# Optimization experiments

Hardware: AMD Instinct MI355X
Metric: run time of the kernel (lower is better)

The kernel has to match this reference:

```python
import jax, jax.numpy as jnp
import numpy as np
from jax import lax

C, K, EMB = 10, 32, 32
B, H, W = 32, 128, 128
DIRS = ((-1, 0), (1, 0), (0, -1), (0, 1))  # up, down, left, right


def _shift(x, dh, dw):
    # shift (B,H,W,...) by (dh,dw) with zero fill; x[b,h,w] <- x[b,h+dh,w+dw]
    pad = [(0, 0), (max(dh, 0), max(-dh, 0)), (max(dw, 0), max(-dw, 0))] + [(0, 0)] * (x.ndim - 3)
    xp = jnp.pad(x, pad)
    h0, w0 = max(-dh, 0), max(-dw, 0)
    return lax.dynamic_slice_in_dim(lax.dynamic_slice_in_dim(xp, h0, x.shape[1], 1), w0, x.shape[2], 2)


def conv(x, w, b):
    y = lax.conv_general_dilated(x, w, (1, 1), 'SAME',
                                 dimension_numbers=('NHWC', 'HWIO', 'NHWC'))
    return y + b


def small_cnn(x, w1, b1, w2, b2, w3, b3):
    x = jax.nn.relu(conv(x, w1, b1))
    x = jax.nn.relu(conv(x, w2, b2))
    return conv(x, w3, b3)


def neighbor_affinity(phi, tau=0.5):
    # phi: (B,H,W,D) -> w: (B,H,W,4) Gaussian feature affinity to 4 neighbors
    ones = jnp.ones(phi.shape[:3] + (1,), phi.dtype)
    ws = []
    for dh, dw in DIRS:
        nb = _shift(phi, dh, dw)
        valid = _shift(ones, dh, dw)[..., 0]
        d2 = jnp.sum((phi - nb) ** 2, axis=-1)
        ws.append(jnp.exp(-d2 / tau) * valid)
    return jnp.stack(ws, axis=-1)


def init_seeds_soft(Bv, Hv, Wv, Kv, dtype=jnp.float32):
    # K seeds on a gh x gw grid; soft assignment by squared distance
    gh = 4
    gw = Kv // gh
    sh = (jnp.arange(gh, dtype=dtype) + 0.5) * (Hv / gh)
    sw = (jnp.arange(gw, dtype=dtype) + 0.5) * (Wv / gw)
    seed_h = jnp.repeat(sh, gw)  # (K,)
    seed_w = jnp.tile(sw, gh)    # (K,)
    hh = jnp.arange(Hv, dtype=dtype)[:, None, None]
    ww = jnp.arange(Wv, dtype=dtype)[None, :, None]
    d2 = (hh - seed_h) ** 2 + (ww - seed_w) ** 2  # (H,W,K)
    sigma2 = (Hv / gh) * (Wv / gw)
    A = jax.nn.softmax(-d2 / sigma2, axis=-1)
    return jnp.broadcast_to(A[None], (Bv, Hv, Wv, Kv))


def soft_message_pass(A, w, beta=2.0):
    # aggregate neighbor assignments weighted by affinity, renormalize over K
    agg = jnp.zeros_like(A)
    for d, (dh, dw) in enumerate(DIRS):
        agg = agg + w[..., d:d + 1] * _shift(A, dh, dw)
    return jax.nn.softmax(beta * agg, axis=-1)


def soft_pool_features(G, A):
    # G:(B,H,W,C), A:(B,H,W,K) -> T:(B,K,1+2+C+4)
    Bv, Hv, Wv, Cv = G.shape
    eps = 1e-6
    mass = jnp.sum(A, axis=(1, 2)) + eps                      # (B,K)
    hh = (jnp.arange(Hv, dtype=G.dtype) + 0.5) / Hv
    ww = (jnp.arange(Wv, dtype=G.dtype) + 0.5) / Wv
    h_c = jnp.einsum('bhwk,h->bk', A, hh) / mass
    w_c = jnp.einsum('bhwk,w->bk', A, ww) / mass
    col = jnp.einsum('bhwk,bhwc->bkc', A, G) / mass[..., None]
    h2 = jnp.einsum('bhwk,h->bk', A, hh ** 2) / mass
    w2 = jnp.einsum('bhwk,w->bk', A, ww ** 2) / mass
    h_sd = jnp.sqrt(jax.nn.relu(h2 - h_c ** 2) + eps)
    w_sd = jnp.sqrt(jax.nn.relu(w2 - w_c ** 2) + eps)
    size = (mass / (Hv * Wv))[..., None]                      # (B,K,1)
    cen = jnp.stack([h_c, w_c], axis=-1)                      # (B,K,2)
    bbox = jnp.stack([h_c - h_sd, h_c + h_sd, w_c - w_sd, w_c + w_sd], axis=-1)
    return jnp.concatenate([size, cen, col, bbox], axis=-1)


def setup_inputs() -> dict:
    key = jax.random.key(0)
    ks = jax.random.split(key, 4)
    X = jax.random.randint(ks[0], (B, H, W), 0, C)
    w1 = jax.random.normal(ks[1], (3, 3, C, 32), jnp.float32) * (1.0 / np.sqrt(9 * C))
    w2 = jax.random.normal(ks[2], (3, 3, 32, 32), jnp.float32) * (1.0 / np.sqrt(9 * 32))
    w3 = jax.random.normal(ks[3], (1, 1, 32, EMB), jnp.float32) * (1.0 / np.sqrt(32))
    return {'X': X, 'w1': w1, 'b1': jnp.zeros((32,), jnp.float32),
            'w2': w2, 'b2': jnp.zeros((32,), jnp.float32),
            'w3': w3, 'b3': jnp.zeros((EMB,), jnp.float32)}


def reference(X, w1, b1, w2, b2, w3, b3):
    G = jax.nn.one_hot(X, C, dtype=jnp.float32)              # (B,H,W,C)
    phi = small_cnn(G, w1, b1, w2, b2, w3, b3)               # (B,H,W,EMB)
    w = neighbor_affinity(phi)                               # (B,H,W,4)
    A = init_seeds_soft(G.shape[0], G.shape[1], G.shape[2], K, G.dtype)
    for _ in range(8):
        A = soft_message_pass(A, w, beta=2.0)
    T = soft_pool_features(G, A)
    return A, T
```

## Files before the change

### kernel.cpp

```cpp
#include <hip/hip_runtime.h>
#include <math.h>

#define HD 128
#define WD 128
#define BB 32
#define KK 32
#define NPIX (BB*HD*WD)

typedef _Float16 f16;
typedef __attribute__((ext_vector_type(8))) _Float16 f16x8;
typedef __attribute__((ext_vector_type(4))) float f32x4;

__device__ __forceinline__ int swz(int row, int g){
  return row*64 + (((g + (row >> 1)) & 3) << 4);
}

__device__ __forceinline__ float xexp2(float x){
#if __has_builtin(__builtin_amdgcn_exp2f)
  return __builtin_amdgcn_exp2f(x);
#else
  return exp2f(x);
#endif
}
__device__ __forceinline__ float xrcp(float x){
#if __has_builtin(__builtin_amdgcn_rcpf)
  return __builtin_amdgcn_rcpf(x);
#else
  return 1.f/x;
#endif
}
__device__ __forceinline__ f16x8 bc8(f16 x){
  f16x8 v;
  #pragma unroll
  for (int j = 0; j < 8; j++) v[j] = x;
  return v;
}

__global__ __launch_bounds__(512, 2) void cnn_kernel(
    const int* __restrict__ X,
    const float* __restrict__ w1, const float* __restrict__ b1,
    const float* __restrict__ w2, const float* __restrict__ b2,
    const float* __restrict__ w3, const float* __restrict__ b3,
    f16* __restrict__ phi)
{
  __shared__ f16 sW1f[9*11*40];
  __shared__ int   sX[20*36];
  __shared__ float sB2[32], sB3[32];
  __shared__ f16 x1[612*32];
  __shared__ f16 w2t[9*32*32];
  __shared__ f16 w3t[32*32];

  const int tid = threadIdx.x;
  const int img = blockIdx.z;
  const int bh0 = blockIdx.y * 16;
  const int bw0 = blockIdx.x * 32;

  for (int i = tid; i < 9*11*32; i += 512) {
    int tap = i / 352, c = (i % 352) >> 5, oc = i & 31;
    float v = (c < 10) ? w1[tap*320 + c*32 + oc] : 0.f;
    if (tap == 4 && c < 10) v += b1[oc];
    sW1f[(tap*11 + c)*40 + oc] = (f16)v;
  }
  for (int i = tid; i < 9*32*32; i += 512) {
    int tap = i >> 10, ic = (i >> 5) & 31, oc = i & 31;
    int off = swz(tap*32 + oc, ic >> 3) + (ic & 7)*2;
    *(f16*)((char*)w2t + off) = (f16)w2[i];
  }
  for (int i = tid; i < 32*32; i += 512) {
    int ic = i >> 5, oe = i & 31;
    int off = swz(oe, ic >> 3) + (ic & 7)*2;
    *(f16*)((char*)w3t + off) = (f16)w3[i];
  }
  if (tid < 32) { sB2[tid] = b2[tid]; sB3[tid] = b3[tid]; }
  for (int i = tid; i < 20*36; i += 512) {
    int ti = i / 36, tj = i % 36;
    int gh = bh0 - 2 + ti, gw = bw0 - 2 + tj;
    sX[i] = (gh >= 0 && gh < HD && gw >= 0 && gw < WD) ? X[(img*HD + gh)*WD + gw] : 10;
  }
  __syncthreads();

  for (int p = tid; p < 612; p += 512) {
    int hr = p / 34, hc = p - hr*34;
    int gh = bh0 + hr - 1, gw = bw0 + hc - 1;
    if (gh >= 0 && gh < HD && gw >= 0 && gw < WD) {
      f16x8 acc[4];
      {
        int c = sX[hr*36 + hc];
        const f16* wr = &sW1f[c*40];
        #pragma unroll
        for (int g = 0; g < 4; g++) acc[g] = *(const f16x8*)(wr + g*8);
      }
      #pragma unroll
      for (int tap = 1; tap < 9; tap++) {
        const int ti = tap/3, tj = tap%3;
        int c = sX[(hr+ti)*36 + hc + tj];
        const f16* wr = &sW1f[(tap*11 + c)*40];
        #pragma unroll
        for (int g = 0; g < 4; g++) acc[g] += *(const f16x8*)(wr + g*8);
      }
      #pragma unroll
      for (int g = 0; g < 4; g++) {
        f16x8 r = acc[g];
        #pragma unroll
        for (int j = 0; j < 8; j++) r[j] = (r[j] > (f16)0.f) ? r[j] : (f16)0.f;
        *(f16x8*)((char*)x1 + swz(p, g)) = r;
      }
    } else {
      f16x8 z;
      #pragma unroll
      for (int j = 0; j < 8; j++) z[j] = (f16)0.f;
      #pragma unroll
      for (int g = 0; g < 4; g++) *(f16x8*)((char*)x1 + swz(p, g)) = z;
    }
  }
  __syncthreads();

  const int lane = tid & 63;
  const int wv   = tid >> 6;
  const int lr   = lane & 15;
  const int kg   = lane >> 4;
  const int mts  = wv * 4;

  int arow0[4];
  #pragma unroll
  for (int q = 0; q < 4; q++) {
    int px = (mts + q)*16 + lr;
    arow0[q] = (px >> 5)*34 + (px & 31);
  }
  float b2v0 = sB2[lr], b2v1 = sB2[lr + 16];
  f32x4 acc[4][2];
  #pragma unroll
  for (int q = 0; q < 4; q++) {
    acc[q][0] = (f32x4){b2v0, b2v0, b2v0, b2v0};
    acc[q][1] = (f32x4){b2v1, b2v1, b2v1, b2v1};
  }
  #pragma unroll
  for (int tap = 0; tap < 9; tap++) {
    const int ti = tap/3, tj = tap%3;
    f16x8 bf0 = *(const f16x8*)((const char*)w2t + swz(tap*32 + lr,      kg));
    f16x8 bf1 = *(const f16x8*)((const char*)w2t + swz(tap*32 + lr + 16, kg));
    #pragma unroll
    for (int q = 0; q < 4; q++) {
      int row = arow0[q] + ti*34 + tj;
      f16x8 af = *(const f16x8*)((const char*)x1 + swz(row, kg));
      acc[q][0] = __builtin_amdgcn_mfma_f32_16x16x32_f16(af, bf0, acc[q][0], 0, 0, 0);
      acc[q][1] = __builtin_amdgcn_mfma_f32_16x16x32_f16(af, bf1, acc[q][1], 0, 0, 0);
    }
  }
  __syncthreads();

  #pragma unroll
  for (int q = 0; q < 4; q++)
    #pragma unroll
    for (int nt = 0; nt < 2; nt++) {
      int oc = nt*16 + lr;
      #pragma unroll
      for (int rg = 0; rg < 4; rg++) {
        int px = (mts + q)*16 + kg*4 + rg;
        int off = swz(px, oc >> 3) + (oc & 7)*2;
        *(f16*)((char*)x1 + off) = (f16)fmaxf(acc[q][nt][rg], 0.f);
      }
    }
  __syncthreads();

  {
    f16x8 cf0 = *(const f16x8*)((const char*)w3t + swz(lr,      kg));
    f16x8 cf1 = *(const f16x8*)((const char*)w3t + swz(lr + 16, kg));
    float b3v0 = sB3[lr], b3v1 = sB3[lr + 16];
    #pragma unroll
    for (int q = 0; q < 4; q++) {
      f16x8 af = *(const f16x8*)((const char*)x1 + swz((mts + q)*16 + lr, kg));
      f32x4 o0 = (f32x4){b3v0, b3v0, b3v0, b3v0};
      f32x4 o1 = (f32x4){b3v1, b3v1, b3v1, b3v1};
      o0 = __builtin_amdgcn_mfma_f32_16x16x32_f16(af, cf0, o0, 0, 0, 0);
      o1 = __builtin_amdgcn_mfma_f32_16x16x32_f16(af, cf1, o1, 0, 0, 0);
      #pragma unroll
      for (int rg = 0; rg < 4; rg++) {
        int px = (mts + q)*16 + kg*4 + rg;
        int gh = bh0 + (px >> 5), gw = bw0 + (px & 31);
        f16* dst = phi + ((size_t)((img*HD + gh)*WD + gw))*32;
        dst[lr]      = (f16)o0[rg];
        dst[lr + 16] = (f16)o1[rg];
      }
    }
  }
}

#define WSCALE 2.8853900817779268f

__device__ __forceinline__ float aff_lds(const f16* __restrict__ sphi, int slot,
                                         f16x8 c0, f16x8 c1, f16x8 c2, f16x8 c3,
                                         bool valid) {
  f16x8 n0 = *(const f16x8*)((const char*)sphi + swz(slot, 0));
  f16x8 n1 = *(const f16x8*)((const char*)sphi + swz(slot, 1));
  f16x8 n2 = *(const f16x8*)((const char*)sphi + swz(slot, 2));
  f16x8 n3 = *(const f16x8*)((const char*)sphi + swz(slot, 3));
  f16x8 d0 = c0 - n0; f16x8 s = d0*d0;
  f16x8 d1 = c1 - n1; s += d1*d1;
  f16x8 d2 = c2 - n2; s += d2*d2;
  f16x8 d3 = c3 - n3; s += d3*d3;
  float d2f = 0.f;
  #pragma unroll
  for (int j = 0; j < 8; j++) d2f += (float)s[j];
  return valid ? WSCALE * xexp2(-WSCALE * d2f) : 0.f;
}

__global__ __launch_bounds__(256, 4) void aff_kernel(const f16* __restrict__ phi, float* __restrict__ wb) {
  __shared__ f16 sphi[612*32];

  const int blk  = blockIdx.x;
  const int tile = blk & 31;
  const int img  = blk >> 5;
  const int th0  = (tile >> 2) * 16;
  const int tw0  = (tile & 3) * 32;
  const size_t ibase = (size_t)img * HD * WD;

  for (int task = threadIdx.x; task < 2448; task += 256) {
    int p = task >> 2, g = task & 3;
    int r = p / 34, c = p - r*34;
    int gh = min(max(th0 - 1 + r, 0), HD-1);
    int gw = min(max(tw0 - 1 + c, 0), WD-1);
    f16x8 v = *(const f16x8*)(phi + (ibase + gh*WD + gw)*32 + g*8);
    *(f16x8*)((char*)sphi + swz(p, g)) = v;
  }
  __syncthreads();

  for (int p2 = threadIdx.x; p2 < 512; p2 += 256) {
    int r2 = p2 >> 5, c2 = p2 & 31;
    int gh = th0 + r2, gw = tw0 + c2;
    int qc = (r2+1)*34 + (c2+1);
    f16x8 c0 = *(const f16x8*)((const char*)sphi + swz(qc, 0));
    f16x8 c1 = *(const f16x8*)((const char*)sphi + swz(qc, 1));
    f16x8 c2v = *(const f16x8*)((const char*)sphi + swz(qc, 2));
    f16x8 c3 = *(const f16x8*)((const char*)sphi + swz(qc, 3));
    float4 out;
    out.x = aff_lds(sphi, qc + 34, c0,c1,c2v,c3, gh < HD-1);
    out.y = aff_lds(sphi, qc - 34, c0,c1,c2v,c3, gh > 0);
    out.z = aff_lds(sphi, qc + 1,  c0,c1,c2v,c3, gw < WD-1);
    out.w = aff_lds(sphi, qc - 1,  c0,c1,c2v,c3, gw > 0);
    ((float4*)wb)[ibase + gh*WD + gw] = out;
  }
}

__device__ __forceinline__ void a0_accum2(float* a, int hh, int ww, float wt) {
  const float C = 0.0028177637517362567f;
  float eh[4], ew[8];
  float sh = 0.f, sw = 0.f;
  const float fh = (float)hh, fw = (float)ww;
  #pragma unroll
  for (int kh = 0; kh < 4; kh++) { float d = fh - (float)(kh*32+16); eh[kh] = xexp2(-d*d*C); sh += eh[kh]; }
  #pragma unroll
  for (int kw = 0; kw < 8; kw++) { float d = fw - (float)(kw*16+8); ew[kw] = xexp2(-d*d*C); sw += ew[kw]; }
  float sc = wt * xrcp(sh * sw);
  #pragma unroll
  for (int kh = 0; kh < 4; kh++) {
    float ehs = eh[kh] * sc;
    #pragma unroll
    for (int kw = 0; kw < 8; kw++) a[kh*8+kw] = fmaf(ehs, ew[kw], a[kh*8+kw]);
  }
}

template<int FIRST, int LAST>
__global__ __launch_bounds__(256, 6) void mp2_kernel(const f16* __restrict__ Ain,
                                                     const float* __restrict__ wb,
                                                     f16* __restrict__ Aout,
                                                     float* __restrict__ AoutF) {
  __shared__ f16 amid[340*32];

  const int blk  = blockIdx.x;
  const int xcd  = blk & 7;
  const int q    = blk >> 3;
  const int img  = xcd + ((q >> 6) << 3);
  const int tile = q & 63;
  const int th0  = (tile >> 2) * 8;
  const int tw0  = (tile & 3) * 32;
  const size_t ibase = (size_t)img * HD * WD;

  for (int p = threadIdx.x; p < 340; p += 256) {
    int r = p / 34, cc = p - r*34;
    int gh = th0 - 1 + r, gw = tw0 - 1 + cc;
    bool inimg = ((unsigned)gh < (unsigned)HD) && ((unsigned)gw < (unsigned)WD);
    int ghc = min(max(gh, 0), HD-1), gwc = min(max(gw, 0), WD-1);
    float4 wd = inimg ? ((const float4*)wb)[ibase + gh*WD + gw] : make_float4(0.f,0.f,0.f,0.f);
    int hu = ghc + ((ghc < HD-1) ? 1 : 0);
    int hd = ghc - ((ghc > 0)    ? 1 : 0);
    int wl = gwc + ((gwc < WD-1) ? 1 : 0);
    int wr = gwc - ((gwc > 0)    ? 1 : 0);

    float s = 0.f;
    f16x8 pe[4];
    if (FIRST) {
      float a[32];
      #pragma unroll
      for (int k = 0; k < 32; k++) a[k] = 0.f;
      a0_accum2(a, hu, gwc, wd.x);
      a0_accum2(a, hd, gwc, wd.y);
      a0_accum2(a, ghc, wl, wd.z);
      a0_accum2(a, ghc, wr, wd.w);
      #pragma unroll
      for (int g = 0; g < 4; g++)
        #pragma unroll
        for (int j = 0; j < 8; j++) { float e = xexp2(a[g*8+j]); s += e; pe[g][j] = (f16)e; }
    } else {
      const f16x8* s0 = (const f16x8*)(Ain + (ibase + (size_t)hu*WD + gwc)*32);
      const f16x8* s1 = (const f16x8*)(Ain + (ibase + (size_t)hd*WD + gwc)*32);
      const f16x8* s2 = (const f16x8*)(Ain + (ibase + (size_t)ghc*WD + wl)*32);
      const f16x8* s3 = (const f16x8*)(Ain + (ibase + (size_t)ghc*WD + wr)*32);
      f16x8 w0 = bc8((f16)wd.x), w1 = bc8((f16)wd.y), w2 = bc8((f16)wd.z), w3 = bc8((f16)wd.w);
      #pragma unroll
      for (int g = 0; g < 4; g++) {
        f16x8 agg = s0[g]*w0 + s1[g]*w1 + s2[g]*w2 + s3[g]*w3;
        #pragma unroll
        for (int j = 0; j < 8; j++) { float e = xexp2((float)agg[j]); s += e; pe[g][j] = (f16)e; }
      }
    }
    f16x8 iv = bc8((f16)xrcp(s));
    #pragma unroll
    for (int g = 0; g < 4; g++)
      *(f16x8*)((char*)amid + swz(p, g)) = pe[g]*iv;
  }
  __syncthreads();

  {
    int r2 = threadIdx.x >> 5, c2 = threadIdx.x & 31;
    int gh = th0 + r2, gw = tw0 + c2;
    int rm = r2 + 1, cm = c2 + 1;
    float4 wd = ((const float4*)wb)[ibase + gh*WD + gw];
    int q0 = (rm + ((gh < HD-1) ? 1 : 0))*34 + cm;
    int q1 = (rm - ((gh > 0)    ? 1 : 0))*34 + cm;
    int q2 = rm*34 + cm + ((gw < WD-1) ? 1 : 0);
    int q3 = rm*34 + cm - ((gw > 0)    ? 1 : 0);
    f16x8 w0 = bc8((f16)wd.x), w1 = bc8((f16)wd.y), w2 = bc8((f16)wd.z), w3 = bc8((f16)wd.w);
    float s = 0.f;
    f16x8 pe[4];
    #pragma unroll
    for (int g = 0; g < 4; g++) {
      f16x8 v0 = *(const f16x8*)((const char*)amid + swz(q0, g));
      f16x8 v1 = *(const f16x8*)((const char*)amid + swz(q1, g));
      f16x8 v2 = *(const f16x8*)((const char*)amid + swz(q2, g));
      f16x8 v3 = *(const f16x8*)((const char*)amid + swz(q3, g));
      f16x8 agg = v0*w0 + v1*w1 + v2*w2 + v3*w3;
      #pragma unroll
      for (int j = 0; j < 8; j++) { float e = xexp2((float)agg[j]); s += e; pe[g][j] = (f16)e; }
    }
    float inv = xrcp(s);
    size_t opix = ibase + (size_t)gh*WD + gw;
    if (LAST) {
      float4* dst = (float4*)(AoutF + opix*32);
      #pragma unroll
      for (int g = 0; g < 4; g++) {
        float4 o1, o2;
        o1.x = (float)pe[g][0]*inv; o1.y = (float)pe[g][1]*inv;
        o1.z = (float)pe[g][2]*inv; o1.w = (float)pe[g][3]*inv;
        o2.x = (float)pe[g][4]*inv; o2.y = (float)pe[g][5]*inv;
        o2.z = (float)pe[g][6]*inv; o2.w = (float)pe[g][7]*inv;
        dst[2*g] = o1; dst[2*g+1] = o2;
      }
    } else {
      f16x8 iv = bc8((f16)inv);
      f16x8* dst = (f16x8*)(Aout + opix*32);
      #pragma unroll
      for (int g = 0; g < 4; g++) dst[g] = pe[g]*iv;
    }
  }
}

__global__ __launch_bounds__(256) void pool1_kernel(const float* __restrict__ A,
                                                    const int* __restrict__ X,
                                                    float* __restrict__ part) {
  const int b = blockIdx.x, cy = blockIdx.y;
  const int k = threadIdx.x & 31, sub = threadIdx.x >> 5;
  const int h = cy*4 + (sub >> 1);
  const int w0 = (sub & 1) * 64;
  const float hh = ((float)h + 0.5f) * (1.f/128.f);
  float s0 = 0.f, sw = 0.f, sw2 = 0.f;
  float col[10];
  #pragma unroll
  for (int c = 0; c < 10; c++) col[c] = 0.f;
  const float* Arow = A + ((size_t)((b*HD + h)*WD + w0))*32 + k;
  const int*   Xrow = X + (b*HD + h)*WD + w0;
  for (int w = 0; w < 64; w++) {
    float a  = Arow[(size_t)w*32];
    float ww = ((float)(w + w0) + 0.5f) * (1.f/128.f);
    s0 += a; sw = fmaf(ww, a, sw); sw2 = fmaf(ww*ww, a, sw2);
    int x = Xrow[w];
    #pragma unroll
    for (int c = 0; c < 10; c++) col[c] += (x == c) ? a : 0.f;
  }
  __shared__ float red[8][32][15];
  float vals[15];
  vals[0] = s0; vals[1] = hh*s0; vals[2] = sw; vals[3] = hh*hh*s0; vals[4] = sw2;
  #pragma unroll
  for (int c = 0; c < 10; c++) vals[5+c] = col[c];
  #pragma unroll
  for (int q = 0; q < 15; q++) red[sub][k][q] = vals[q];
  __syncthreads();
  if (sub == 0) {
    #pragma unroll
    for (int q = 0; q < 15; q++) {
      float v = 0.f;
      #pragma unroll
      for (int s2 = 0; s2 < 8; s2++) v += red[s2][k][q];
      part[(((size_t)b*32 + cy)*32 + k)*15 + q] = v;
    }
  }
}

__global__ __launch_bounds__(256) void pool2_kernel(const float* __restrict__ part,
                                                    float* __restrict__ T) {
  const int t = blockIdx.x * 256 + threadIdx.x;
  if (t >= BB*KK) return;
  const int b = t >> 5, k = t & 31;
  float s[15];
  #pragma unroll
  for (int q = 0; q < 15; q++) s[q] = 0.f;
  for (int cy = 0; cy < 32; cy++) {
    const float* p = part + (((size_t)b*32 + cy)*32 + k)*15;
    #pragma unroll
    for (int q = 0; q < 15; q++) s[q] += p[q];
  }
  float mass = s[0] + 1e-6f;
  float inv  = 1.f / mass;
  float h_c = s[1]*inv, w_c = s[2]*inv, h2 = s[3]*inv, w2 = s[4]*inv;
  float h_sd = sqrtf(fmaxf(h2 - h_c*h_c, 0.f) + 1e-6f);
  float w_sd = sqrtf(fmaxf(w2 - w_c*w_c, 0.f) + 1e-6f);
  float* o = T + (size_t)t*17;
  o[0] = mass * (1.f/16384.f);
  o[1] = h_c; o[2] = w_c;
  #pragma unroll
  for (int c = 0; c < 10; c++) o[3+c] = s[5+c]*inv;
  o[13] = h_c - h_sd; o[14] = h_c + h_sd; o[15] = w_c - w_sd; o[16] = w_c + w_sd;
}

extern "C" void kernel_launch(void* const* d_in, const int* in_sizes, int n_in,
                              void* d_out, int out_size, void* d_ws, size_t ws_size,
                              hipStream_t stream) {
  const int*   X  = (const int*)d_in[0];
  const float* w1 = (const float*)d_in[1];
  const float* b1 = (const float*)d_in[2];
  const float* w2 = (const float*)d_in[3];
  const float* b2 = (const float*)d_in[4];
  const float* w3 = (const float*)d_in[5];
  const float* b3 = (const float*)d_in[6];

  float* out   = (float*)d_out;
  float* A_out = out;
  float* T_out = out + (size_t)NPIX * KK;

  char*  ws   = (char*)d_ws;
  f16*   bufA = (f16*)ws;
  float* wb   = (float*)(ws + (size_t)32*1024*1024);
  f16*   bufB = (f16*)(ws + (size_t)40*1024*1024);
  float* part = (float*)ws;

  f16* phi = bufB;
  cnn_kernel<<<dim3(WD/32, HD/16, BB), 512, 0, stream>>>(X, w1, b1, w2, b2, w3, b3, phi);
  aff_kernel<<<1024, 256, 0, stream>>>(phi, wb);

  mp2_kernel<1,0><<<2048, 256, 0, stream>>>(nullptr, wb, bufA, nullptr);
  mp2_kernel<0,0><<<2048, 256, 0, stream>>>(bufA, wb, bufB, nullptr);
  mp2_kernel<0,0><<<2048, 256, 0, stream>>>(bufB, wb, bufA, nullptr);
  mp2_kernel<0,1><<<2048, 256, 0, stream>>>(bufA, wb, nullptr, A_out);

  pool1_kernel<<<dim3(BB, 32), 256, 0, stream>>>(A_out, X, part);
  pool2_kernel<<<(BB*KK + 255)/256, 256, 0, stream>>>(part, T_out);
}
```

Before: 271.5 us.

## Store message-pass assignments in planar fp16 layout with separate fp32 conversion

Splits the 32-channel assignment tensor into four planes of 8 fp16 channels each, so adjacent threads read and write adjacent 16-byte chunks in the message-pass kernels. The last message-pass step now writes fp16 like the others. A new conversion kernel expands that result into the fp32 A output, and the pooling kernel reads the smaller fp16 planar buffer instead of the fp32 output. The aim is better coalescing and less pooling read traffic. The cost is an extra kernel launch, an extra pass over the data, and fp16 rounding of the final A values.

```diff
diff --git a/kernel.cpp b/kernel.cpp
--- a/kernel.cpp
+++ b/kernel.cpp
@@ -6,6 +6,7 @@
 #define BB 32
 #define KK 32
 #define NPIX (BB*HD*WD)
+#define PLANE ((size_t)NPIX*8)
 
 typedef _Float16 f16;
 typedef __attribute__((ext_vector_type(8))) _Float16 f16x8;
@@ -260,11 +261,10 @@
   }
 }
 
-template<int FIRST, int LAST>
+template<int FIRST>
 __global__ __launch_bounds__(256, 6) void mp2_kernel(const f16* __restrict__ Ain,
                                                      const float* __restrict__ wb,
-                                                     f16* __restrict__ Aout,
-                                                     float* __restrict__ AoutF) {
+                                                     f16* __restrict__ Aout) {
   __shared__ f16 amid[340*32];
 
   const int blk  = blockIdx.x;
@@ -302,14 +302,19 @@
         #pragma unroll
         for (int j = 0; j < 8; j++) { float e = xexp2(a[g*8+j]); s += e; pe[g][j] = (f16)e; }
     } else {
-      const f16x8* s0 = (const f16x8*)(Ain + (ibase + (size_t)hu*WD + gwc)*32);
-      const f16x8* s1 = (const f16x8*)(Ain + (ibase + (size_t)hd*WD + gwc)*32);
-      const f16x8* s2 = (const f16x8*)(Ain + (ibase + (size_t)ghc*WD + wl)*32);
-      const f16x8* s3 = (const f16x8*)(Ain + (ibase + (size_t)ghc*WD + wr)*32);
+      const size_t iu_ = ibase + (size_t)hu*WD + gwc;
+      const size_t id_ = ibase + (size_t)hd*WD + gwc;
+      const size_t il_ = ibase + (size_t)ghc*WD + wl;
+      const size_t ir_ = ibase + (size_t)ghc*WD + wr;
       f16x8 w0 = bc8((f16)wd.x), w1 = bc8((f16)wd.y), w2 = bc8((f16)wd.z), w3 = bc8((f16)wd.w);
       #pragma unroll
       for (int g = 0; g < 4; g++) {
-        f16x8 agg = s0[g]*w0 + s1[g]*w1 + s2[g]*w2 + s3[g]*w3;
+        const f16* pg = Ain + (size_t)g*PLANE;
+        f16x8 v0 = *(const f16x8*)(pg + iu_*8);
+        f16x8 v1 = *(const f16x8*)(pg + id_*8);
+        f16x8 v2 = *(const f16x8*)(pg + il_*8);
+        f16x8 v3 = *(const f16x8*)(pg + ir_*8);
+        f16x8 agg = v0*w0 + v1*w1 + v2*w2 + v3*w3;
         #pragma unroll
         for (int j = 0; j < 8; j++) { float e = xexp2((float)agg[j]); s += e; pe[g][j] = (f16)e; }
       }
@@ -343,29 +348,27 @@
       #pragma unroll
       for (int j = 0; j < 8; j++) { float e = xexp2((float)agg[j]); s += e; pe[g][j] = (f16)e; }
     }
-    float inv = xrcp(s);
+    f16x8 iv = bc8((f16)xrcp(s));
     size_t opix = ibase + (size_t)gh*WD + gw;
-    if (LAST) {
-      float4* dst = (float4*)(AoutF + opix*32);
-      #pragma unroll
-      for (int g = 0; g < 4; g++) {
-        float4 o1, o2;
-        o1.x = (float)pe[g][0]*inv; o1.y = (float)pe[g][1]*inv;
-        o1.z = (float)pe[g][2]*inv; o1.w = (float)pe[g][3]*inv;
-        o2.x = (float)pe[g][4]*inv; o2.y = (float)pe[g][5]*inv;
-        o2.z = (float)pe[g][6]*inv; o2.w = (float)pe[g][7]*inv;
-        dst[2*g] = o1; dst[2*g+1] = o2;
-      }
-    } else {
-      f16x8 iv = bc8((f16)inv);
-      f16x8* dst = (f16x8*)(Aout + opix*32);
-      #pragma unroll
-      for (int g = 0; g < 4; g++) dst[g] = pe[g]*iv;
-    }
-  }
-}
-
-__global__ __launch_bounds__(256) void pool1_kernel(const float* __restrict__ A,
+    #pragma unroll
+    for (int g = 0; g < 4; g++)
+      *(f16x8*)(Aout + (size_t)g*PLANE + opix*8) = pe[g]*iv;
+  }
+}
+
+__global__ __launch_bounds__(256) void conv_kernel(const f16* __restrict__ Ap,
+                                                   float* __restrict__ Aout) {
+  const int t = blockIdx.x * 256 + threadIdx.x;
+  const int px = t >> 2, g = t & 3;
+  f16x8 v = *(const f16x8*)(Ap + (size_t)g*PLANE + (size_t)px*8);
+  float4 o0, o1;
+  o0.x = (float)v[0]; o0.y = (float)v[1]; o0.z = (float)v[2]; o0.w = (float)v[3];
+  o1.x = (float)v[4]; o1.y = (float)v[5]; o1.z = (float)v[6]; o1.w = (float)v[7];
+  float4* dst = (float4*)(Aout + (size_t)px*32 + g*8);
+  dst[0] = o0; dst[1] = o1;
+}
+
+__global__ __launch_bounds__(256) void pool1_kernel(const f16* __restrict__ Ap,
                                                     const int* __restrict__ X,
                                                     float* __restrict__ part) {
   const int b = blockIdx.x, cy = blockIdx.y;
@@ -377,10 +380,10 @@
   float col[10];
   #pragma unroll
   for (int c = 0; c < 10; c++) col[c] = 0.f;
-  const float* Arow = A + ((size_t)((b*HD + h)*WD + w0))*32 + k;
-  const int*   Xrow = X + (b*HD + h)*WD + w0;
+  const f16* pl = Ap + (size_t)(k >> 3)*PLANE + ((size_t)((b*HD + h)*WD + w0))*8 + (k & 7);
+  const int* Xrow = X + (b*HD + h)*WD + w0;
   for (int w = 0; w < 64; w++) {
-    float a  = Arow[(size_t)w*32];
+    float a  = (float)pl[w*8];
     float ww = ((float)(w + w0) + 0.5f) * (1.f/128.f);
     s0 += a; sw = fmaf(ww, a, sw); sw2 = fmaf(ww*ww, a, sw2);
     int x = Xrow[w];
@@ -449,19 +452,20 @@
 
   char*  ws   = (char*)d_ws;
   f16*   bufA = (f16*)ws;
-  float* wb   = (float*)(ws + (size_t)32*1024*1024);
-  f16*   bufB = (f16*)(ws + (size_t)40*1024*1024);
+  f16*   bufB = (f16*)(ws + (size_t)32*1024*1024);
+  float* wb   = (float*)(ws + (size_t)64*1024*1024);
   float* part = (float*)ws;
 
   f16* phi = bufB;
   cnn_kernel<<<dim3(WD/32, HD/16, BB), 512, 0, stream>>>(X, w1, b1, w2, b2, w3, b3, phi);
   aff_kernel<<<1024, 256, 0, stream>>>(phi, wb);
 
-  mp2_kernel<1,0><<<2048, 256, 0, stream>>>(nullptr, wb, bufA, nullptr);
-  mp2_kernel<0,0><<<2048, 256, 0, stream>>>(bufA, wb, bufB, nullptr);
-  mp2_kernel<0,0><<<2048, 256, 0, stream>>>(bufB, wb, bufA, nullptr);
-  mp2_kernel<0,1><<<2048, 256, 0, stream>>>(bufA, wb, nullptr, A_out);
-
-  pool1_kernel<<<dim3(BB, 32), 256, 0, stream>>>(A_out, X, part);
+  mp2_kernel<1><<<2048, 256, 0, stream>>>(nullptr, wb, bufA);
+  mp2_kernel<0><<<2048, 256, 0, stream>>>(bufA, wb, bufB);
+  mp2_kernel<0><<<2048, 256, 0, stream>>>(bufB, wb, bufA);
+  mp2_kernel<0><<<2048, 256, 0, stream>>>(bufA, wb, bufB);
+
+  conv_kernel<<<NPIX*4/256, 256, 0, stream>>>(bufB, A_out);
+  pool1_kernel<<<dim3(BB, 32), 256, 0, stream>>>(bufB, X, part);
   pool2_kernel<<<(BB*KK + 255)/256, 256, 0, stream>>>(part, T_out);
 }
```

Result: no change. 269.8 us (-0.6%).
